# Kernel tuning notes

Measured on AMD Instinct MI355X. Metric: run time of the kernel, lower is better.

## Reference

```python
import jax, jax.numpy as jnp
import numpy as np

B, N, FIN, H, F = 8, 1024, 256, 8, 64
NEG_SLOPE = 0.2


def setup_inputs() -> dict:
    key = jax.random.key(0)
    k = jax.random.split(key, 6)
    x = jax.random.normal(k[0], (B, N, FIN), dtype=jnp.float32)
    adj_mask = jax.random.randint(k[1], (B, N, N), 0, 2, dtype=jnp.int32)
    edge_prior = jax.random.normal(k[2], (B, N, N), dtype=jnp.float32)
    # params (xavier-style scales)
    W = jax.random.normal(k[3], (FIN, H * F), dtype=jnp.float32) * np.sqrt(2.0 / (FIN + H * F))
    a_left = jax.random.normal(k[4], (H, F), dtype=jnp.float32) * np.sqrt(2.0 / (1 + F))
    a_right = jax.random.normal(k[5], (H, F), dtype=jnp.float32) * np.sqrt(2.0 / (1 + F))
    edge_scale = jnp.float32(0.05)
    return {"x": x, "adj_mask": adj_mask, "edge_prior": edge_prior,
            "W": W, "a_left": a_left, "a_right": a_right, "edge_scale": edge_scale}


def reference(x, adj_mask, edge_prior, W, a_left, a_right, edge_scale):
    b, n, _ = x.shape
    h = (x @ W).reshape(b, n, H, F)                      # [B,N,H,F]
    e_left = jnp.einsum('bnhf,hf->bnh', h, a_left)       # [B,N,H]
    e_right = jnp.einsum('bnhf,hf->bnh', h, a_right)     # [B,N,H]
    e = jax.nn.leaky_relu(e_left[:, :, None, :] + e_right[:, None, :, :],
                          negative_slope=NEG_SLOPE)      # [B,N,N,H]
    e = e + edge_scale * edge_prior[..., None]
    e = jnp.where((adj_mask == 0)[..., None], -jnp.inf, e)
    alpha = jax.nn.softmax(e, axis=2)                    # softmax over neighbors j
    h_new = jnp.einsum('bijh,bjhf->bihf', alpha, h)      # [B,N,H,F]
    return h_new.reshape(b, n, H * F)                    # concat=True
```

## Files before the change

### kernel.cpp

```cpp
#include <hip/hip_runtime.h>
#include <hip/hip_bf16.h>

#define B_ 8
#define N_ 1024
#define FIN_ 256
#define H_ 8
#define F_ 64
#define HF_ 512
#define BN_ 8192
#define LOG2E 1.4426950408889634f

using bf16x8 = __attribute__((ext_vector_type(8))) short;
using f32x4  = __attribute__((ext_vector_type(4))) float;
using i32x4  = __attribute__((ext_vector_type(4))) int;

__device__ __forceinline__ short f2bf(float x) {
  __hip_bfloat16 b = __float2bfloat16(x);
  return *reinterpret_cast<short*>(&b);
}
__device__ __forceinline__ float bf2f(short s) {
  union { unsigned u; float f; } v;
  v.u = ((unsigned)(unsigned short)s) << 16;
  return v.f;
}
__device__ __forceinline__ bf16x8 cvtCE(f32x4 pa, f32x4 pb, i32x4 ma, i32x4 mb, float es) {
  bf16x8 o;
#pragma unroll
  for (int e = 0; e < 4; e++) {
    o[e]     = f2bf(ma[e] != 0 ? es * pa[e] : -1e30f);
    o[e + 4] = f2bf(mb[e] != 0 ? es * pb[e] : -1e30f);
  }
  return o;
}

__global__ __launch_bounds__(256) void k_cvt(
    const float* __restrict__ x, const float* __restrict__ W,
    short* __restrict__ xb, short* __restrict__ Wt) {
  const int bid = blockIdx.x;
  if (bid < 1024) {
    const int idx = (bid * 256 + threadIdx.x) * 8;
    f32x4 a = *(const f32x4*)(x + idx);
    f32x4 b = *(const f32x4*)(x + idx + 4);
    bf16x8 o;
    o[0]=f2bf(a[0]); o[1]=f2bf(a[1]); o[2]=f2bf(a[2]); o[3]=f2bf(a[3]);
    o[4]=f2bf(b[0]); o[5]=f2bf(b[1]); o[6]=f2bf(b[2]); o[7]=f2bf(b[3]);
    *(bf16x8*)(xb + idx) = o;
  } else {
    const int idx = (bid - 1024) * 256 + threadIdx.x;
    const int f = idx >> 8, c = idx & 255;
    Wt[f * FIN_ + c] = f2bf(W[c * HF_ + f]);
  }
}

__global__ __launch_bounds__(256) void k_h(
    const short* __restrict__ Wt, const short* __restrict__ xb,
    const float* __restrict__ aL, const float* __restrict__ aR,
    short* __restrict__ hAg, float* __restrict__ el_t, float* __restrict__ er_t) {
  const int nt = blockIdx.x;
  const int h  = blockIdx.y;
  const int w  = threadIdx.x >> 6;
  const int l  = threadIdx.x & 63;
  const int lr = l & 15, lk = l >> 4;
  const int n0 = nt * 64;
  const int fbase = h * 64 + w * 16;

  f32x4 acc[4] = {};
  const short* arow = Wt + (fbase + lr) * FIN_ + lk * 8;

#pragma unroll
  for (int k0 = 0; k0 < FIN_; k0 += 32) {
    bf16x8 a = *(const bf16x8*)(arow + k0);
#pragma unroll
    for (int nf = 0; nf < 4; nf++) {
      bf16x8 bb = *(const bf16x8*)(xb + (size_t)(n0 + nf * 16 + lr) * FIN_ + k0 + lk * 8);
      acc[nf] = __builtin_amdgcn_mfma_f32_16x16x32_bf16(a, bb, acc[nf], 0, 0, 0);
    }
  }

  __shared__ short sT[64][72];
  __shared__ float sEl[4][64], sEr[4][64];
  float al[4], ar[4];
#pragma unroll
  for (int r = 0; r < 4; r++) {
    const int fl = w * 16 + lk * 4 + r;
    al[r] = aL[h * F_ + fl];
    ar[r] = aR[h * F_ + fl];
  }
#pragma unroll
  for (int nf = 0; nf < 4; nf++) {
    const int nl = nf * 16 + lr;
#pragma unroll
    for (int r = 0; r < 4; r++)
      sT[w * 16 + lk * 4 + r][nl] = f2bf(acc[nf][r]);
    float pl = acc[nf][0]*al[0] + acc[nf][1]*al[1] + acc[nf][2]*al[2] + acc[nf][3]*al[3];
    float pr = acc[nf][0]*ar[0] + acc[nf][1]*ar[1] + acc[nf][2]*ar[2] + acc[nf][3]*ar[3];
    pl += __shfl_xor(pl, 16); pl += __shfl_xor(pl, 32);
    pr += __shfl_xor(pr, 16); pr += __shfl_xor(pr, 32);
    if (lk == 0) { sEl[w][nl] = pl; sEr[w][nl] = pr; }
  }
  __syncthreads();
  if (threadIdx.x < 64) {
    const int n = threadIdx.x;
    el_t[h * BN_ + n0 + n] = (sEl[0][n] + sEl[1][n] + sEl[2][n] + sEl[3][n]) * LOG2E;
    er_t[h * BN_ + n0 + n] = (sEr[0][n] + sEr[1][n] + sEr[2][n] + sEr[3][n]) * LOG2E;
  }
  const int b8h = (nt >> 4) * 8 + h;
  const int jb  = (nt & 15) * 2;
#pragma unroll
  for (int gi = 0; gi < 2; gi++) {
    const int g   = threadIdx.x * 2 + gi;
    const int jsl = g >> 8, ff = (g >> 6) & 3, gl = g & 63;
    const int glr = gl & 15, glk = gl >> 4;
    bf16x8 v = *(const bf16x8*)(&sT[ff * 16 + glr][jsl * 32 + glk * 8]);
    *(bf16x8*)(hAg + (((size_t)b8h * 32 + jb + jsl) * 4 + ff) * 512 + gl * 8) = v;
  }
}

#define PREF_G(sn, Hd, E0d, E1d)                                      \
  {                                                                   \
    const short* hs_ = hW + (size_t)(sn) * 2048;                      \
    Hd[0] = *(const bf16x8*)(hs_);                                    \
    Hd[1] = *(const bf16x8*)(hs_ + 512);                              \
    Hd[2] = *(const bf16x8*)(hs_ + 1024);                             \
    Hd[3] = *(const bf16x8*)(hs_ + 1536);                             \
    E0d   = *(const f32x4*)(erp + (sn) * 32);                         \
    E1d   = *(const f32x4*)(erp + (sn) * 32 + 4);                     \
  }

#define PREF_C(sn, C0d, C1d)                                          \
  {                                                                   \
    const int gi_ = (((sn) * 4 + lk) ^ xsw) * 8;                      \
    C0d = *(const bf16x8*)(cbl0 + gi_);                               \
    C1d = *(const bf16x8*)(cbl1 + gi_);                               \
  }

#define COMP2(Hu, C0u, C1u, E0u, E1u)                                          \
  {                                                                            \
    bf16x8 pfA, pfB;                                                           \
    _Pragma("unroll")                                                          \
    for (int q = 0; q < 4; q++) {                                              \
      const float e0 = E0u[q], e1 = E1u[q];                                    \
      float sA  = el0 + e0, sA2 = el0 + e1;                                    \
      float sB  = el1 + e0, sB2 = el1 + e1;                                    \
      float vA  = fmaf(0.6f, sA,  bf2f(C0u[q]));                               \
      vA  = fmaf(0.4f, fabsf(sA),  vA);                                        \
      float vA2 = fmaf(0.6f, sA2, bf2f(C0u[q + 4]));                           \
      vA2 = fmaf(0.4f, fabsf(sA2), vA2);                                       \
      float vB  = fmaf(0.6f, sB,  bf2f(C1u[q]));                               \
      vB  = fmaf(0.4f, fabsf(sB),  vB);                                        \
      float vB2 = fmaf(0.6f, sB2, bf2f(C1u[q + 4]));                           \
      vB2 = fmaf(0.4f, fabsf(sB2), vB2);                                       \
      float x1_, x2_, x3_, x4_;                                                \
      asm("v_exp_f32 %0, %1" : "=v"(x1_) : "v"(vA));                           \
      asm("v_exp_f32 %0, %1" : "=v"(x2_) : "v"(vA2));                          \
      asm("v_exp_f32 %0, %1" : "=v"(x3_) : "v"(vB));                           \
      asm("v_exp_f32 %0, %1" : "=v"(x4_) : "v"(vB2));                          \
      pfA[q] = f2bf(x1_); pfA[q + 4] = f2bf(x2_);                              \
      pfB[q] = f2bf(x3_); pfB[q + 4] = f2bf(x4_);                              \
    }                                                                          \
    __builtin_amdgcn_s_setprio(1);                                             \
    accSA   = __builtin_amdgcn_mfma_f32_16x16x32_bf16(ones, pfA, accSA, 0,0,0);\
    accSB   = __builtin_amdgcn_mfma_f32_16x16x32_bf16(ones, pfB, accSB, 0,0,0);\
    accA[0] = __builtin_amdgcn_mfma_f32_16x16x32_bf16(Hu[0], pfA, accA[0],0,0,0);\
    accB[0] = __builtin_amdgcn_mfma_f32_16x16x32_bf16(Hu[0], pfB, accB[0],0,0,0);\
    accA[1] = __builtin_amdgcn_mfma_f32_16x16x32_bf16(Hu[1], pfA, accA[1],0,0,0);\
    accB[1] = __builtin_amdgcn_mfma_f32_16x16x32_bf16(Hu[1], pfB, accB[1],0,0,0);\
    accA[2] = __builtin_amdgcn_mfma_f32_16x16x32_bf16(Hu[2], pfA, accA[2],0,0,0);\
    accB[2] = __builtin_amdgcn_mfma_f32_16x16x32_bf16(Hu[2], pfB, accB[2],0,0,0);\
    accA[3] = __builtin_amdgcn_mfma_f32_16x16x32_bf16(Hu[3], pfA, accA[3],0,0,0);\
    accB[3] = __builtin_amdgcn_mfma_f32_16x16x32_bf16(Hu[3], pfB, accB[3],0,0,0);\
    __builtin_amdgcn_s_setprio(0);                                             \
  }

__global__ __launch_bounds__(256, 2) void k_attn(
    const short* __restrict__ hAg, const float* __restrict__ el_t,
    const float* __restrict__ er_t, const float* __restrict__ prior,
    const int* __restrict__ mask, const float* __restrict__ esp,
    float* __restrict__ out) {
  const int bid = blockIdx.x;
  const int b  = bid & 7;
  const int hp = (bid >> 3) & 1;
  const int it = bid >> 4;
  const int t  = threadIdx.x;
  const int h  = hp * 4 + (t >> 6);
  const int l  = t & 63;
  const int lr = l & 15, lk = l >> 4;
  const int i0 = it * 32;
  const size_t bn = (size_t)b * N_;
  const float es = esp[0] * LOG2E;

  __shared__ short cbuf[33 * 1024];

  {
    const int srow = t >> 3;
    const int g0   = t & 7;
    const int sw   = srow & 7;
    const size_t grow = (bn + i0 + srow) * (size_t)N_;
    const float* pg = prior + grow;
    const int*   mg = mask  + grow;
#pragma unroll
    for (int k = 0; k < 16; k++) {
      const int g = g0 + 8 * k;
      f32x4 p0 = *(const f32x4*)(pg + g * 8), p1 = *(const f32x4*)(pg + g * 8 + 4);
      i32x4 m0 = *(const i32x4*)(mg + g * 8), m1 = *(const i32x4*)(mg + g * 8 + 4);
      *(bf16x8*)(&cbuf[srow * 1024 + (g ^ sw) * 8]) = cvtCE(p0, p1, m0, m1, es);
    }
  }

  const float el0 = el_t[h * BN_ + bn + i0 + lr];
  const float el1 = el_t[h * BN_ + bn + i0 + 16 + lr];
  const float* erp = er_t + h * BN_ + bn + lk * 8;
  const short* hW  = hAg + (size_t)(b * 8 + h) * 65536 + l * 8;
  const short* cbl0 = cbuf + lr * 1024;
  const short* cbl1 = cbuf + (16 + lr) * 1024;
  const int xsw = lr & 7;

  bf16x8 HA[4], HB[4], cA0, cA1, cB0, cB1;
  f32x4 eA0, eA1, eB0, eB1;

  PREF_G(0, HA, eA0, eA1);
  PREF_G(1, HB, eB0, eB1);

  f32x4 accA[4] = {}, accB[4] = {};
  f32x4 accSA = {}, accSB = {};
  bf16x8 ones;
#pragma unroll
  for (int e = 0; e < 8; e++) ones[e] = (short)0x3F80;

  __syncthreads();
  PREF_C(0, cA0, cA1);
  PREF_C(1, cB0, cB1);
  __builtin_amdgcn_sched_barrier(0);

  for (int s = 0; s < 32; s += 2) {
    COMP2(HA, cA0, cA1, eA0, eA1);
    __builtin_amdgcn_sched_barrier(0);
    PREF_G(s + 2, HA, eA0, eA1);
    PREF_C(s + 2, cA0, cA1);
    __builtin_amdgcn_sched_barrier(0);
    COMP2(HB, cB0, cB1, eB0, eB1);
    __builtin_amdgcn_sched_barrier(0);
    PREF_G(s + 3, HB, eB0, eB1);
    PREF_C(s + 3, cB0, cB1);
    __builtin_amdgcn_sched_barrier(0);
  }

  const float invA = 1.0f / accSA[0];
  const float invB = 1.0f / accSB[0];
  const size_t rowA = bn + i0 + lr;
  const size_t rowB = rowA + 16;
#pragma unroll
  for (int ff = 0; ff < 4; ff++) {
    f32x4 va = accA[ff], vb = accB[ff];
    va[0]*=invA; va[1]*=invA; va[2]*=invA; va[3]*=invA;
    vb[0]*=invB; vb[1]*=invB; vb[2]*=invB; vb[3]*=invB;
    *(f32x4*)(out + rowA * HF_ + h * 64 + ff * 16 + lk * 4) = va;
    *(f32x4*)(out + rowB * HF_ + h * 64 + ff * 16 + lk * 4) = vb;
  }
}

extern "C" void kernel_launch(void* const* d_in, const int* in_sizes, int n_in,
                              void* d_out, int out_size, void* d_ws, size_t ws_size,
                              hipStream_t stream) {
  const float* x     = (const float*)d_in[0];
  const int*   adj   = (const int*)  d_in[1];
  const float* prior = (const float*)d_in[2];
  const float* W     = (const float*)d_in[3];
  const float* aL    = (const float*)d_in[4];
  const float* aR    = (const float*)d_in[5];
  const float* es    = (const float*)d_in[6];
  float* out = (float*)d_out;

  char* ws = (char*)d_ws;
  short* hAg  = (short*)ws;
  short* xb   = (short*)(ws + 8u  * 1024 * 1024);
  short* Wt   = (short*)(ws + 12u * 1024 * 1024);
  float* el_t = (float*)(ws + 12u * 1024 * 1024 + 262144);
  float* er_t = (float*)(ws + 12u * 1024 * 1024 + 524288);

  hipLaunchKernelGGL(k_cvt, dim3(1536), dim3(256), 0, stream, x, W, xb, Wt);
  hipLaunchKernelGGL(k_h,   dim3(128, 8), dim3(256), 0, stream,
                     Wt, xb, aL, aR, hAg, el_t, er_t);
  hipLaunchKernelGGL(k_attn, dim3(512), dim3(256), 0, stream,
                     hAg, el_t, er_t, prior, adj, es, out);
}
```

Measured before the change: 63.78 us.

## Double-buffer prior/mask staging in LDS and cover all eight heads per block

The attention kernel now uses 512-thread blocks covering all eight heads, so the prior/mask rows for a 32-row tile are read once per block instead of twice. Those rows are staged in four 256-column chunks in a double-buffered LDS buffer, and the next chunk's global loads overlap the MFMA work on the current chunk. The per-block LDS footprint shrinks, but the grid halves to 256 blocks, which lowers parallelism, and each chunk adds a barrier. Nontemporal loads and stores are also used for the streamed prior, mask and output.

```diff
diff --git a/kernel.cpp b/kernel.cpp
--- a/kernel.cpp
+++ b/kernel.cpp
@@ -127,11 +127,31 @@
     E1d   = *(const f32x4*)(erp + (sn) * 32 + 4);                     \
   }
 
-#define PREF_C(sn, C0d, C1d)                                          \
+#define PREF_C(cbp, js, C0d, C1d)                                     \
   {                                                                   \
-    const int gi_ = (((sn) * 4 + lk) ^ xsw) * 8;                      \
-    C0d = *(const bf16x8*)(cbl0 + gi_);                               \
-    C1d = *(const bf16x8*)(cbl1 + gi_);                               \
+    const int gi_ = ((((js) * 4 + lk) ^ xsw) * 8);                    \
+    C0d = *(const bf16x8*)((cbp) + lr * 256 + gi_);                   \
+    C1d = *(const bf16x8*)((cbp) + 4096 + lr * 256 + gi_);            \
+  }
+
+#define STAGE_LOAD(ch)                                                \
+  {                                                                   \
+    const float* pp_ = rowp + (ch) * 256;                             \
+    const int*   mm_ = rowm + (ch) * 256;                             \
+    sp0 = __builtin_nontemporal_load((const f32x4*)(pp_));            \
+    sp1 = __builtin_nontemporal_load((const f32x4*)(pp_ + 4));        \
+    sp2 = __builtin_nontemporal_load((const f32x4*)(pp_ + 8));        \
+    sp3 = __builtin_nontemporal_load((const f32x4*)(pp_ + 12));       \
+    sm0 = __builtin_nontemporal_load((const i32x4*)(mm_));            \
+    sm1 = __builtin_nontemporal_load((const i32x4*)(mm_ + 4));        \
+    sm2 = __builtin_nontemporal_load((const i32x4*)(mm_ + 8));        \
+    sm3 = __builtin_nontemporal_load((const i32x4*)(mm_ + 12));       \
+  }
+
+#define STAGE_WRITE(cbw)                                              \
+  {                                                                   \
+    *(bf16x8*)((cbw) + rbase + g0s) = cvtCE(sp0, sp1, sm0, sm1, es);  \
+    *(bf16x8*)((cbw) + rbase + g1s) = cvtCE(sp2, sp3, sm2, sm3, es);  \
   }
 
 #define COMP2(Hu, C0u, C1u, E0u, E1u)                                          \
@@ -172,54 +192,42 @@
     __builtin_amdgcn_s_setprio(0);                                             \
   }
 
-__global__ __launch_bounds__(256, 2) void k_attn(
+__global__ __launch_bounds__(512, 2) void k_attn(
     const short* __restrict__ hAg, const float* __restrict__ el_t,
     const float* __restrict__ er_t, const float* __restrict__ prior,
     const int* __restrict__ mask, const float* __restrict__ esp,
     float* __restrict__ out) {
   const int bid = blockIdx.x;
   const int b  = bid & 7;
-  const int hp = (bid >> 3) & 1;
-  const int it = bid >> 4;
+  const int it = bid >> 3;
   const int t  = threadIdx.x;
-  const int h  = hp * 4 + (t >> 6);
+  const int h  = t >> 6;
   const int l  = t & 63;
   const int lr = l & 15, lk = l >> 4;
   const int i0 = it * 32;
   const size_t bn = (size_t)b * N_;
   const float es = esp[0] * LOG2E;
 
-  __shared__ short cbuf[33 * 1024];
-
-  {
-    const int srow = t >> 3;
-    const int g0   = t & 7;
-    const int sw   = srow & 7;
-    const size_t grow = (bn + i0 + srow) * (size_t)N_;
-    const float* pg = prior + grow;
-    const int*   mg = mask  + grow;
-#pragma unroll
-    for (int k = 0; k < 16; k++) {
-      const int g = g0 + 8 * k;
-      f32x4 p0 = *(const f32x4*)(pg + g * 8), p1 = *(const f32x4*)(pg + g * 8 + 4);
-      i32x4 m0 = *(const i32x4*)(mg + g * 8), m1 = *(const i32x4*)(mg + g * 8 + 4);
-      *(bf16x8*)(&cbuf[srow * 1024 + (g ^ sw) * 8]) = cvtCE(p0, p1, m0, m1, es);
-    }
-  }
+  __shared__ short cbuf[2][8192];
+
+  const int r    = t >> 4;
+  const int sub  = t & 15;
+  const int rbase = r * 256;
+  const int g0s  = ((sub * 2) ^ (r & 7)) * 8;
+  const int g1s  = ((sub * 2 + 1) ^ (r & 7)) * 8;
+  const float* rowp = prior + (bn + i0 + r) * (size_t)N_ + sub * 16;
+  const int*   rowm = mask  + (bn + i0 + r) * (size_t)N_ + sub * 16;
+  f32x4 sp0, sp1, sp2, sp3;
+  i32x4 sm0, sm1, sm2, sm3;
 
   const float el0 = el_t[h * BN_ + bn + i0 + lr];
   const float el1 = el_t[h * BN_ + bn + i0 + 16 + lr];
   const float* erp = er_t + h * BN_ + bn + lk * 8;
   const short* hW  = hAg + (size_t)(b * 8 + h) * 65536 + l * 8;
-  const short* cbl0 = cbuf + lr * 1024;
-  const short* cbl1 = cbuf + (16 + lr) * 1024;
   const int xsw = lr & 7;
 
   bf16x8 HA[4], HB[4], cA0, cA1, cB0, cB1;
   f32x4 eA0, eA1, eB0, eB1;
-
-  PREF_G(0, HA, eA0, eA1);
-  PREF_G(1, HB, eB0, eB1);
 
   f32x4 accA[4] = {}, accB[4] = {};
   f32x4 accSA = {}, accSB = {};
@@ -227,22 +235,39 @@
 #pragma unroll
   for (int e = 0; e < 8; e++) ones[e] = (short)0x3F80;
 
+  STAGE_LOAD(0);
+  __builtin_amdgcn_sched_barrier(0);
+  STAGE_WRITE(&cbuf[0][0]);
+  PREF_G(0, HA, eA0, eA1);
+  PREF_G(1, HB, eB0, eB1);
   __syncthreads();
-  PREF_C(0, cA0, cA1);
-  PREF_C(1, cB0, cB1);
-  __builtin_amdgcn_sched_barrier(0);
-
-  for (int s = 0; s < 32; s += 2) {
+  PREF_C(&cbuf[0][0], 0, cA0, cA1);
+  PREF_C(&cbuf[0][0], 1, cB0, cB1);
+
+  for (int ch = 0; ch < 4; ++ch) {
+    const int s0 = ch * 8;
+    const short* cbc = &cbuf[ch & 1][0];
+    short*       cbn = &cbuf[(ch + 1) & 1][0];
+    if (ch < 3) {
+      STAGE_LOAD(ch + 1);
+      __builtin_amdgcn_sched_barrier(0);
+    }
+    COMP2(HA, cA0, cA1, eA0, eA1);  PREF_G(s0 + 2, HA, eA0, eA1);  PREF_C(cbc, 2, cA0, cA1);
+    COMP2(HB, cB0, cB1, eB0, eB1);  PREF_G(s0 + 3, HB, eB0, eB1);  PREF_C(cbc, 3, cB0, cB1);
+    COMP2(HA, cA0, cA1, eA0, eA1);  PREF_G(s0 + 4, HA, eA0, eA1);  PREF_C(cbc, 4, cA0, cA1);
+    COMP2(HB, cB0, cB1, eB0, eB1);  PREF_G(s0 + 5, HB, eB0, eB1);  PREF_C(cbc, 5, cB0, cB1);
+    COMP2(HA, cA0, cA1, eA0, eA1);  PREF_G(s0 + 6, HA, eA0, eA1);  PREF_C(cbc, 6, cA0, cA1);
+    COMP2(HB, cB0, cB1, eB0, eB1);  PREF_G(s0 + 7, HB, eB0, eB1);  PREF_C(cbc, 7, cB0, cB1);
     COMP2(HA, cA0, cA1, eA0, eA1);
-    __builtin_amdgcn_sched_barrier(0);
-    PREF_G(s + 2, HA, eA0, eA1);
-    PREF_C(s + 2, cA0, cA1);
-    __builtin_amdgcn_sched_barrier(0);
+    { const int sn_ = (s0 + 8 > 31) ? 31 : s0 + 8; PREF_G(sn_, HA, eA0, eA1); }
     COMP2(HB, cB0, cB1, eB0, eB1);
-    __builtin_amdgcn_sched_barrier(0);
-    PREF_G(s + 3, HB, eB0, eB1);
-    PREF_C(s + 3, cB0, cB1);
-    __builtin_amdgcn_sched_barrier(0);
+    { const int sn_ = (s0 + 9 > 31) ? 31 : s0 + 9; PREF_G(sn_, HB, eB0, eB1); }
+    if (ch < 3) {
+      STAGE_WRITE(cbn);
+      __syncthreads();
+      PREF_C(cbn, 0, cA0, cA1);
+      PREF_C(cbn, 1, cB0, cB1);
+    }
   }
 
   const float invA = 1.0f / accSA[0];
@@ -254,8 +279,8 @@
     f32x4 va = accA[ff], vb = accB[ff];
     va[0]*=invA; va[1]*=invA; va[2]*=invA; va[3]*=invA;
     vb[0]*=invB; vb[1]*=invB; vb[2]*=invB; vb[3]*=invB;
-    *(f32x4*)(out + rowA * HF_ + h * 64 + ff * 16 + lk * 4) = va;
-    *(f32x4*)(out + rowB * HF_ + h * 64 + ff * 16 + lk * 4) = vb;
+    __builtin_nontemporal_store(va, (f32x4*)(out + rowA * HF_ + h * 64 + ff * 16 + lk * 4));
+    __builtin_nontemporal_store(vb, (f32x4*)(out + rowB * HF_ + h * 64 + ff * 16 + lk * 4));
   }
 }
 
@@ -281,6 +306,6 @@
   hipLaunchKernelGGL(k_cvt, dim3(1536), dim3(256), 0, stream, x, W, xb, Wt);
   hipLaunchKernelGGL(k_h,   dim3(128, 8), dim3(256), 0, stream,
                      Wt, xb, aL, aR, hAg, el_t, er_t);
-  hipLaunchKernelGGL(k_attn, dim3(512), dim3(256), 0, stream,
+  hipLaunchKernelGGL(k_attn, dim3(256), dim3(512), 0, stream,
                      hAg, el_t, er_t, prior, adj, es, out);
 }
```

Result: slower. 72.16 us (+13.1%).
